# Kernel optimization log

Measured on AMD Instinct MI355X. Metric: run time of the kernel, lower is better.

## Reference

```python
import jax, jax.numpy as jnp
import numpy as np
import math

C = 256
N_HEAD = 8
GROUPS = 32
EPS = 1e-5


def group_norm(x, scale, bias, groups=GROUPS, eps=EPS):
    # x: [B, C, H, W]
    b, c, h, w = x.shape
    xg = x.reshape(b, groups, c // groups, h, w)
    mean = xg.mean(axis=(2, 3, 4), keepdims=True)
    var = xg.var(axis=(2, 3, 4), keepdims=True)
    xg = (xg - mean) * jax.lax.rsqrt(var + eps)
    x = xg.reshape(b, c, h, w)
    return x * scale[None, :, None, None] + bias[None, :, None, None]


def setup_inputs() -> dict:
    key = jax.random.key(0)
    ks = jax.random.split(key, 8)
    B, H, W = 8, 32, 32
    inp = {
        "input_q": jax.random.normal(ks[0], (B, C, H, W), dtype=jnp.float32),
        "input_kv": jax.random.normal(ks[1], (B, C, H, W), dtype=jnp.float32),
        # GroupNorm affine params (torch default: weight=1, bias=0)
        "gq_scale": jnp.ones((C,), jnp.float32),
        "gq_bias": jnp.zeros((C,), jnp.float32),
        "gkv_scale": jnp.ones((C,), jnp.float32),
        "gkv_bias": jnp.zeros((C,), jnp.float32),
        # 1x1 convs as [out, in] matrices
        "Wq": jax.random.normal(ks[2], (C, C), dtype=jnp.float32) / math.sqrt(C),
        "Wkv": jax.random.normal(ks[3], (2 * C, C), dtype=jnp.float32) / math.sqrt(C),
        "Wout": jax.random.normal(ks[4], (C, C), dtype=jnp.float32) / math.sqrt(C),
        "bout": jnp.zeros((C,), jnp.float32),
    }
    return inp


def reference(input_q, input_kv, gq_scale, gq_bias, gkv_scale, gkv_bias, Wq, Wkv, Wout, bout):
    b, c, h, w = input_q.shape
    n = N_HEAD
    d = c // n

    norm_q = group_norm(input_q, gq_scale, gq_bias)
    query = jnp.einsum('oc,bchw->bohw', Wq, norm_q).reshape(b, n, d, h, w)

    norm_kv = group_norm(input_kv, gkv_scale, gkv_bias)
    kv = jnp.einsum('oc,bchw->bohw', Wkv, norm_kv).reshape(b, n, 2 * d, h, w)
    key, value = kv[:, :, :d], kv[:, :, d:]

    attn = jnp.einsum('bnchw,bncyx->bnhwyx', query, key) / math.sqrt(c)
    attn = jax.nn.softmax(attn.reshape(b, n, h, w, h * w), axis=-1)
    attn = attn.reshape(b, n, h, w, h, w)

    out = jnp.einsum('bnhwyx,bncyx->bnchw', attn, value).reshape(b, c, h, w)
    out = jnp.einsum('oc,bchw->bohw', Wout, out) + bout[None, :, None, None]
    return out + input_q
```

## Files before the change

### kernel.cpp

```cpp
#include <hip/hip_runtime.h>
#include <hip/hip_bf16.h>
#include <math.h>
#include <string.h>

#define NB 8
#define NC 256
#define HWSZ 1024
#define NHEAD 8
#define DHEAD 32
#define NGRP 32
#define CPG 8
#define EPSV 1e-5f

typedef float f32x4 __attribute__((ext_vector_type(4)));
typedef short bf16x8 __attribute__((ext_vector_type(8)));

__device__ __forceinline__ unsigned pk2(float a, float b) {
    __hip_bfloat162 h = __float22bfloat162_rn(make_float2(a, b));
    unsigned r;
    memcpy(&r, &h, sizeof(r));
    return r;
}
__device__ __forceinline__ unsigned pk2t(float a, float b) {
    unsigned ua = __float_as_uint(a), ub = __float_as_uint(b);
    return (ua >> 16) | (ub & 0xFFFF0000u);
}
__device__ __forceinline__ unsigned short f2bf(float x) {
    __hip_bfloat16 h = __float2bfloat16(x);
    unsigned short r;
    memcpy(&r, &h, sizeof(r));
    return r;
}
__device__ __forceinline__ float ex2(float x) { return __builtin_amdgcn_exp2f(x); }

__device__ __forceinline__ void gload_lds16(const void* g, void* l) {
    __builtin_amdgcn_global_load_lds(
        (const __attribute__((address_space(1))) unsigned int*)g,
        (__attribute__((address_space(3))) unsigned int*)l, 16, 0, 0);
}

__global__ void prep_kernel(const float* __restrict__ xq,
                            const float* __restrict__ xkv,
                            float* __restrict__ stats,
                            const float* __restrict__ Wq,
                            const float* __restrict__ Wkv,
                            const float* __restrict__ Wout,
                            unsigned short* __restrict__ wqb,
                            unsigned short* __restrict__ wkvb,
                            unsigned short* __restrict__ woutb) {
    if (blockIdx.x < 512) {
        int idx = blockIdx.x;
        int which = idx >> 8;
        int b = (idx >> 5) & 7;
        int g = idx & 31;
        const float* x = which ? xkv : xq;
        const float4* xb = (const float4*)(x + ((size_t)(b * NC + g * CPG)) * HWSZ);
        float s = 0.f, ss = 0.f;
        for (int i = threadIdx.x; i < (CPG * HWSZ) / 4; i += 256) {
            float4 v = xb[i];
            s += v.x + v.y + v.z + v.w;
            ss += v.x * v.x + v.y * v.y + v.z * v.z + v.w * v.w;
        }
        #pragma unroll
        for (int off = 32; off > 0; off >>= 1) {
            s += __shfl_down(s, off);
            ss += __shfl_down(ss, off);
        }
        __shared__ float red[8];
        int wid = threadIdx.x >> 6;
        if ((threadIdx.x & 63) == 0) { red[wid * 2] = s; red[wid * 2 + 1] = ss; }
        __syncthreads();
        if (threadIdx.x == 0) {
            float S = red[0] + red[2] + red[4] + red[6];
            float SS = red[1] + red[3] + red[5] + red[7];
            float mean = S * (1.f / (CPG * HWSZ));
            float var = SS * (1.f / (CPG * HWSZ)) - mean * mean;
            stats[idx * 2] = mean;
            stats[idx * 2 + 1] = rsqrtf(var + EPSV);
        }
    } else {
        int gid = (blockIdx.x - 512) * 256 + threadIdx.x;
        int i0 = gid * 8;
        const float* src; unsigned short* dst; int off; float sc = 1.f;
        if (i0 < 65536)       { src = Wq;   dst = wqb;   off = i0;          sc = 0.0625f * 1.44269504088896f; }
        else if (i0 < 196608) { src = Wkv;  dst = wkvb;  off = i0 - 65536; }
        else                  { src = Wout; dst = woutb; off = i0 - 196608; }
        float4 v0 = *(const float4*)&src[off];
        float4 v1 = *(const float4*)&src[off + 4];
        uint4 o;
        o.x = pk2(v0.x * sc, v0.y * sc); o.y = pk2(v0.z * sc, v0.w * sc);
        o.z = pk2(v1.x * sc, v1.y * sc); o.w = pk2(v1.z * sc, v1.w * sc);
        *(uint4*)&dst[off] = o;
    }
}

__global__ __launch_bounds__(256) void qkv_gemm_kernel(
        const unsigned short* __restrict__ wqb,
        const unsigned short* __restrict__ wkvb,
        const float* __restrict__ xq, const float* __restrict__ xkv,
        const float* __restrict__ stats,
        const float* __restrict__ sq, const float* __restrict__ bq,
        const float* __restrict__ skv, const float* __restrict__ bkv,
        unsigned short* __restrict__ qbuf,
        unsigned short* __restrict__ kbuf,
        unsigned short* __restrict__ vbuf) {
    __shared__ unsigned short Bs[64 * 256];
    const int tid = threadIdx.x;
    const int l16 = tid & 15, g = (tid >> 4) & 3, w = tid >> 6;
    const int y = blockIdx.y;
    const bool isQ = y < 4;
    const int o0 = (isQ ? y : y - 4) * 64;
    const size_t prow0 = (size_t)blockIdx.x * 64;
    const int b = (int)(prow0 >> 10);
    const int pp = (int)(prow0 & 1023);

    const float* X  = (isQ ? xq : xkv) + (size_t)b * NC * HWSZ + pp;
    const float* st = stats + (isQ ? 0 : 512) + b * 64;
    const float* sc = isQ ? sq : skv;
    const float* bi = isQ ? bq : bkv;

    const unsigned short* Asrc = (isQ ? wqb : wkvb)
                               + ((size_t)o0 + 16 * w + l16) * NC;
    bf16x8 af[8];
    #pragma unroll
    for (int kk = 0; kk < 8; ++kk)
        af[kk] = *(const bf16x8*)&Asrc[(kk * 4 + g) << 3];

    const int cq = tid >> 4, pq = tid & 15;
    #pragma unroll
    for (int j = 0; j < 4; ++j) {
        int cb = cq * 4 + j * 64;
        int grp = cb >> 3;
        float mean = st[grp * 2], rstd = st[grp * 2 + 1];
        float mm[4][4];
        #pragma unroll
        for (int u = 0; u < 4; ++u) {
            int c = cb + u;
            float4 v = *(const float4*)&X[(size_t)c * HWSZ + pq * 4];
            float a = rstd * sc[c];
            float bbv = bi[c] - mean * a;
            mm[u][0] = v.x * a + bbv; mm[u][1] = v.y * a + bbv;
            mm[u][2] = v.z * a + bbv; mm[u][3] = v.w * a + bbv;
        }
        #pragma unroll
        for (int v2 = 0; v2 < 4; ++v2) {
            int row = pq * 4 + v2;
            int ds = row * 256 + ((((cb >> 3) ^ (row & 7))) << 3) + (cb & 7);
            uint2 s2;
            s2.x = pk2(mm[0][v2], mm[1][v2]);
            s2.y = pk2(mm[2][v2], mm[3][v2]);
            *(uint2*)&Bs[ds] = s2;
        }
    }
    __syncthreads();

    f32x4 acc[4] = {};
    const int asw = l16 & 7;
    #pragma unroll
    for (int kk = 0; kk < 8; ++kk) {
        const int koff = ((kk * 4 + g) ^ asw) << 3;
        #pragma unroll
        for (int j = 0; j < 4; ++j) {
            bf16x8 bfr = *(const bf16x8*)&Bs[(j * 16 + l16) * 256 + koff];
            acc[j] = __builtin_amdgcn_mfma_f32_16x16x32_bf16(af[kk], bfr, acc[j], 0, 0, 0);
        }
    }

    if (isQ) {
        int ob_ = o0 + 16 * w + 4 * g;
        int n = ob_ >> 5, d0 = ob_ & 31;
        unsigned short* dst = qbuf + ((size_t)(b * NHEAD + n) * HWSZ) * DHEAD + d0;
        #pragma unroll
        for (int j = 0; j < 4; ++j) {
            int p = pp + 16 * j + l16;
            uint2 st2;
            st2.x = pk2(acc[j][0], acc[j][1]);
            st2.y = pk2(acc[j][2], acc[j][3]);
            *(uint2*)&dst[(size_t)p * DHEAD] = st2;
        }
    } else {
        int n = o0 >> 6;
        int d0 = 16 * (w & 1) + 4 * g;
        if (w < 2) {
            unsigned short* dst = kbuf + ((size_t)(b * NHEAD + n) * HWSZ) * DHEAD + d0;
            #pragma unroll
            for (int j = 0; j < 4; ++j) {
                int p = pp + 16 * j + l16;
                uint2 st2;
                st2.x = pk2(acc[j][0], acc[j][1]);
                st2.y = pk2(acc[j][2], acc[j][3]);
                *(uint2*)&dst[(size_t)p * DHEAD] = st2;
            }
        } else {
            unsigned short* dst = vbuf + ((size_t)(b * NHEAD + n) * DHEAD + d0) * HWSZ;
            #pragma unroll
            for (int j = 0; j < 4; ++j) {
                int slot = ((l16 >> 2) << 3) + ((j & 1) << 2) + (l16 & 3);
                int p = pp + 32 * (j >> 1) + slot;
                #pragma unroll
                for (int r = 0; r < 4; ++r)
                    dst[(size_t)r * HWSZ + p] = f2bf(acc[j][r]);
            }
        }
    }
}

__global__ __launch_bounds__(256) void out_gemm_kernel(
        const unsigned short* __restrict__ Abase,
        const unsigned short* __restrict__ Bbase,
        const float* __restrict__ bias_out,
        const float* __restrict__ resid,
        float* __restrict__ out0) {
    __shared__ unsigned short Bs[64 * 256];
    const int tid = threadIdx.x;
    const int l16 = tid & 15, g = (tid >> 4) & 3, w = tid >> 6;
    const int o0 = blockIdx.y * 64;
    const size_t prow0 = (size_t)blockIdx.x * 64;

    const unsigned short* Asrc = Abase + (prow0 + 16 * w + l16) * NC;
    bf16x8 af[8];
    #pragma unroll
    for (int kk = 0; kk < 8; ++kk)
        af[kk] = *(const bf16x8*)&Asrc[(kk * 4 + g) << 3];

    const unsigned short* Bsrc = Bbase + (size_t)o0 * NC;
    #pragma unroll
    for (int it = 0; it < 4; ++it) {
        int idx = tid + it * 256;
        int row = idx >> 4, seg = idx & 15;
        #pragma unroll
        for (int h = 0; h < 2; ++h) {
            int sg = seg * 2 + h;
            int ds = row * 256 + ((sg ^ (row & 7)) << 3);
            *(uint4*)&Bs[ds] = *(const uint4*)&Bsrc[(size_t)row * NC + sg * 8];
        }
    }
    __syncthreads();

    f32x4 acc[4] = {};
    const int asw = l16 & 7;
    #pragma unroll
    for (int kk = 0; kk < 8; ++kk) {
        const int koff = ((kk * 4 + g) ^ asw) << 3;
        #pragma unroll
        for (int j = 0; j < 4; ++j) {
            bf16x8 b = *(const bf16x8*)&Bs[(j * 16 + l16) * 256 + koff];
            acc[j] = __builtin_amdgcn_mfma_f32_16x16x32_bf16(af[kk], b, acc[j], 0, 0, 0);
        }
    }
    const int b = (int)(prow0 >> 10);
    const int pp = (int)(prow0 & 1023);
    int p_b = pp + 16 * w + 4 * g;
    #pragma unroll
    for (int j = 0; j < 4; ++j) {
        int o = o0 + 16 * j + l16;
        float bo = bias_out[o];
        size_t off = ((size_t)b * NC + o) * HWSZ + p_b;
        float4 rs = *(const float4*)&resid[off];
        float4 vst = make_float4(acc[j][0] + bo + rs.x, acc[j][1] + bo + rs.y,
                                 acc[j][2] + bo + rs.z, acc[j][3] + bo + rs.w);
        *(float4*)&out0[off] = vst;
    }
}

__global__ __launch_bounds__(256) void attn_mfma_kernel(
        const unsigned short* __restrict__ qb,
        const unsigned short* __restrict__ kb,
        const unsigned short* __restrict__ vb,
        unsigned short* __restrict__ ob) {
    __shared__ unsigned short KV[3][4096];
    const int tid = threadIdx.x;
    const int w = tid >> 6, lane = tid & 63;
    const int l16 = lane & 15, g = lane >> 4;
    const int F = blockIdx.y * 16 + blockIdx.x;
    const int bn = (F & 7) * 8 + (F >> 7);
    const int qblk = (F >> 3) & 15;
    const int qp = qblk * 64 + w * 16 + l16;

    bf16x8 qf = *(const bf16x8*)(qb + ((size_t)bn * HWSZ + qp) * DHEAD + g * 8);

    const int kr = tid >> 2, ks = tid & 3;
    const unsigned short* ksrc = kb + (size_t)bn * HWSZ * DHEAD
                               + (size_t)kr * DHEAD + ((ks ^ (kr & 3)) << 3);
    const int vr = tid >> 3, vs = tid & 7;
    const unsigned short* vsrc = vb + (size_t)bn * DHEAD * HWSZ
                               + (size_t)vr * HWSZ + ((vs ^ (vr & 7)) << 3);
    unsigned short* lk = &KV[0][0] + w * 512;
    unsigned short* lv = &KV[0][2048] + w * 512;

#define STAGE(t) do {                                                        \
        int b3_ = (t) % 3; int ti_ = (t) & 15;                               \
        gload_lds16(ksrc + (size_t)ti_ * 64 * DHEAD, lk + b3_ * 4096);       \
        gload_lds16(vsrc + (size_t)ti_ * 64,         lv + b3_ * 4096);       \
    } while (0)

    f32x4 acc0 = {0.f, 0.f, 0.f, 0.f}, acc1 = {0.f, 0.f, 0.f, 0.f};
    f32x4 accl = {0.f, 0.f, 0.f, 0.f};
    const f32x4 z = {0.f, 0.f, 0.f, 0.f};

    const unsigned on2 = 0x3F803F80u;
    uint4 onev = make_uint4(on2, on2, on2, on2);
    bf16x8 ones;
    memcpy(&ones, &onev, sizeof(ones));

    const int ksw  = (g ^ (l16 & 3)) << 3;
    const int vsw0 = ((g)     ^ (l16 & 7)) << 3;
    const int vsw1 = ((4 + g) ^ (l16 & 7)) << 3;

    STAGE(0);
    STAGE(1);

    #pragma unroll
    for (int t = 0; t < 16; ++t) {
        const int cur = t % 3;
        asm volatile("s_waitcnt vmcnt(2)" ::: "memory");
        __builtin_amdgcn_s_barrier();
        STAGE(t + 2);

        const unsigned short* Kb = &KV[cur][0];
        const unsigned short* Vb = &KV[cur][2048];
        bf16x8 ka0 = *(const bf16x8*)&Kb[(l16)      * 32 + ksw];
        bf16x8 ka1 = *(const bf16x8*)&Kb[(16 + l16) * 32 + ksw];
        bf16x8 ka2 = *(const bf16x8*)&Kb[(32 + l16) * 32 + ksw];
        bf16x8 ka3 = *(const bf16x8*)&Kb[(48 + l16) * 32 + ksw];

        __builtin_amdgcn_s_setprio(1);
        f32x4 s0 = __builtin_amdgcn_mfma_f32_16x16x32_bf16(ka0, qf, z, 0, 0, 0);
        f32x4 s1 = __builtin_amdgcn_mfma_f32_16x16x32_bf16(ka1, qf, z, 0, 0, 0);
        f32x4 s2 = __builtin_amdgcn_mfma_f32_16x16x32_bf16(ka2, qf, z, 0, 0, 0);
        f32x4 s3 = __builtin_amdgcn_mfma_f32_16x16x32_bf16(ka3, qf, z, 0, 0, 0);
        __builtin_amdgcn_s_setprio(0);

        float p00 = ex2(s0[0]), p01 = ex2(s0[1]);
        float p02 = ex2(s0[2]), p03 = ex2(s0[3]);
        float p10 = ex2(s1[0]), p11 = ex2(s1[1]);
        float p12 = ex2(s1[2]), p13 = ex2(s1[3]);
        float p20 = ex2(s2[0]), p21 = ex2(s2[1]);
        float p22 = ex2(s2[2]), p23 = ex2(s2[3]);
        float p30 = ex2(s3[0]), p31 = ex2(s3[1]);
        float p32 = ex2(s3[2]), p33 = ex2(s3[3]);

        uint4 pwa, pwb;
        pwa.x = pk2t(p00, p01); pwa.y = pk2t(p02, p03);
        pwa.z = pk2t(p10, p11); pwa.w = pk2t(p12, p13);
        pwb.x = pk2t(p20, p21); pwb.y = pk2t(p22, p23);
        pwb.z = pk2t(p30, p31); pwb.w = pk2t(p32, p33);
        bf16x8 pf0, pf1;
        memcpy(&pf0, &pwa, sizeof(pf0));
        memcpy(&pf1, &pwb, sizeof(pf1));

        bf16x8 va0 = *(const bf16x8*)&Vb[(l16)      * 64 + vsw0];
        bf16x8 va1 = *(const bf16x8*)&Vb[(l16)      * 64 + vsw1];
        bf16x8 vb0 = *(const bf16x8*)&Vb[(16 + l16) * 64 + vsw0];
        bf16x8 vb1 = *(const bf16x8*)&Vb[(16 + l16) * 64 + vsw1];

        __builtin_amdgcn_s_setprio(1);
        acc0 = __builtin_amdgcn_mfma_f32_16x16x32_bf16(va0, pf0, acc0, 0, 0, 0);
        acc0 = __builtin_amdgcn_mfma_f32_16x16x32_bf16(va1, pf1, acc0, 0, 0, 0);
        acc1 = __builtin_amdgcn_mfma_f32_16x16x32_bf16(vb0, pf0, acc1, 0, 0, 0);
        acc1 = __builtin_amdgcn_mfma_f32_16x16x32_bf16(vb1, pf1, acc1, 0, 0, 0);
        accl = __builtin_amdgcn_mfma_f32_16x16x32_bf16(ones, pf0, accl, 0, 0, 0);
        accl = __builtin_amdgcn_mfma_f32_16x16x32_bf16(ones, pf1, accl, 0, 0, 0);
        __builtin_amdgcn_s_setprio(0);
    }
#undef STAGE

    float invl = 1.f / accl[0];

    const int b = bn >> 3, n = bn & 7;
    unsigned short* dst = ob + ((size_t)b * HWSZ + qp) * NC + n * DHEAD;
    uint2 st0, st1;
    st0.x = pk2(acc0[0] * invl, acc0[1] * invl);
    st0.y = pk2(acc0[2] * invl, acc0[3] * invl);
    st1.x = pk2(acc1[0] * invl, acc1[1] * invl);
    st1.y = pk2(acc1[2] * invl, acc1[3] * invl);
    *(uint2*)&dst[4 * g]      = st0;
    *(uint2*)&dst[16 + 4 * g] = st1;
}

extern "C" void kernel_launch(void* const* d_in, const int* in_sizes, int n_in,
                              void* d_out, int out_size, void* d_ws, size_t ws_size,
                              hipStream_t stream) {
    const float* input_q  = (const float*)d_in[0];
    const float* input_kv = (const float*)d_in[1];
    const float* gq_scale = (const float*)d_in[2];
    const float* gq_bias  = (const float*)d_in[3];
    const float* gkv_scale = (const float*)d_in[4];
    const float* gkv_bias  = (const float*)d_in[5];
    const float* Wq   = (const float*)d_in[6];
    const float* Wkv  = (const float*)d_in[7];
    const float* Wout = (const float*)d_in[8];
    const float* bout = (const float*)d_in[9];
    float* out = (float*)d_out;

    char* ws = (char*)d_ws;
    float* stats = (float*)ws;
    unsigned short* wqb   = (unsigned short*)(ws + 16384);
    unsigned short* wkvb  = (unsigned short*)(ws + 16384 + 131072);
    unsigned short* woutb = (unsigned short*)(ws + 16384 + 131072 + 262144);
    const size_t MB = 1024 * 1024;
    unsigned short* qbuf = (unsigned short*)(ws + 1 * MB);
    unsigned short* kbuf = (unsigned short*)(ws + 5 * MB);
    unsigned short* vbuf = (unsigned short*)(ws + 9 * MB);
    unsigned short* obuf = (unsigned short*)(ws + 13 * MB);

    prep_kernel<<<640, 256, 0, stream>>>(input_q, input_kv, stats,
                                         Wq, Wkv, Wout, wqb, wkvb, woutb);
    qkv_gemm_kernel<<<dim3(128, 12), 256, 0, stream>>>(
        wqb, wkvb, input_q, input_kv, stats,
        gq_scale, gq_bias, gkv_scale, gkv_bias, qbuf, kbuf, vbuf);
    attn_mfma_kernel<<<dim3(16, 64), 256, 0, stream>>>(qbuf, kbuf, vbuf, obuf);
    out_gemm_kernel<<<dim3(128, 4), 256, 0, stream>>>(obuf, woutb, bout, input_q, out);
}
```

Baseline: 48.98 us.

## Pre-normalize inputs to channel-group-packed bf16 in prep kernel

```diff
diff --git a/kernel.cpp b/kernel.cpp
--- a/kernel.cpp
+++ b/kernel.cpp
@@ -41,10 +41,15 @@
 
 __global__ void prep_kernel(const float* __restrict__ xq,
                             const float* __restrict__ xkv,
-                            float* __restrict__ stats,
+                            const float* __restrict__ gq_scale,
+                            const float* __restrict__ gq_bias,
+                            const float* __restrict__ gkv_scale,
+                            const float* __restrict__ gkv_bias,
                             const float* __restrict__ Wq,
                             const float* __restrict__ Wkv,
                             const float* __restrict__ Wout,
+                            unsigned short* __restrict__ xnq,
+                            unsigned short* __restrict__ xnkv,
                             unsigned short* __restrict__ wqb,
                             unsigned short* __restrict__ wkvb,
                             unsigned short* __restrict__ woutb) {
@@ -66,7 +71,7 @@
             s += __shfl_down(s, off);
             ss += __shfl_down(ss, off);
         }
-        __shared__ float red[8];
+        __shared__ float red[10];
         int wid = threadIdx.x >> 6;
         if ((threadIdx.x & 63) == 0) { red[wid * 2] = s; red[wid * 2 + 1] = ss; }
         __syncthreads();
@@ -75,8 +80,35 @@
             float SS = red[1] + red[3] + red[5] + red[7];
             float mean = S * (1.f / (CPG * HWSZ));
             float var = SS * (1.f / (CPG * HWSZ)) - mean * mean;
-            stats[idx * 2] = mean;
-            stats[idx * 2 + 1] = rsqrtf(var + EPSV);
+            red[8] = mean;
+            red[9] = rsqrtf(var + EPSV);
+        }
+        __syncthreads();
+        const float mean = red[8], rstd = red[9];
+        const float* scp = which ? gkv_scale : gq_scale;
+        const float* bip = which ? gkv_bias : gq_bias;
+        float a[8], bb[8];
+        #pragma unroll
+        for (int u = 0; u < 8; ++u) {
+            int c = g * 8 + u;
+            a[u] = rstd * scp[c];
+            bb[u] = bip[c] - mean * a[u];
+        }
+        const int p0 = threadIdx.x * 4;
+        f32x4 rowv[8];
+        #pragma unroll
+        for (int u = 0; u < 8; ++u)
+            rowv[u] = *(const f32x4*)&x[((size_t)(b * NC + g * 8 + u)) * HWSZ + p0];
+        unsigned short* xt = (which ? xnkv : xnq)
+                           + (((size_t)b * NGRP + g) * HWSZ) * 8;
+        #pragma unroll
+        for (int pi = 0; pi < 4; ++pi) {
+            uint4 o;
+            o.x = pk2(rowv[0][pi] * a[0] + bb[0], rowv[1][pi] * a[1] + bb[1]);
+            o.y = pk2(rowv[2][pi] * a[2] + bb[2], rowv[3][pi] * a[3] + bb[3]);
+            o.z = pk2(rowv[4][pi] * a[4] + bb[4], rowv[5][pi] * a[5] + bb[5]);
+            o.w = pk2(rowv[6][pi] * a[6] + bb[6], rowv[7][pi] * a[7] + bb[7]);
+            *(uint4*)&xt[(size_t)(p0 + pi) * 8] = o;
         }
     } else {
         int gid = (blockIdx.x - 512) * 256 + threadIdx.x;
@@ -97,10 +129,8 @@
 __global__ __launch_bounds__(256) void qkv_gemm_kernel(
         const unsigned short* __restrict__ wqb,
         const unsigned short* __restrict__ wkvb,
-        const float* __restrict__ xq, const float* __restrict__ xkv,
-        const float* __restrict__ stats,
-        const float* __restrict__ sq, const float* __restrict__ bq,
-        const float* __restrict__ skv, const float* __restrict__ bkv,
+        const unsigned short* __restrict__ xnq,
+        const unsigned short* __restrict__ xnkv,
         unsigned short* __restrict__ qbuf,
         unsigned short* __restrict__ kbuf,
         unsigned short* __restrict__ vbuf) {
@@ -114,11 +144,6 @@
     const int b = (int)(prow0 >> 10);
     const int pp = (int)(prow0 & 1023);
 
-    const float* X  = (isQ ? xq : xkv) + (size_t)b * NC * HWSZ + pp;
-    const float* st = stats + (isQ ? 0 : 512) + b * 64;
-    const float* sc = isQ ? sq : skv;
-    const float* bi = isQ ? bq : bkv;
-
     const unsigned short* Asrc = (isQ ? wqb : wkvb)
                                + ((size_t)o0 + 16 * w + l16) * NC;
     bf16x8 af[8];
@@ -126,31 +151,14 @@
     for (int kk = 0; kk < 8; ++kk)
         af[kk] = *(const bf16x8*)&Asrc[(kk * 4 + g) << 3];
 
-    const int cq = tid >> 4, pq = tid & 15;
-    #pragma unroll
-    for (int j = 0; j < 4; ++j) {
-        int cb = cq * 4 + j * 64;
-        int grp = cb >> 3;
-        float mean = st[grp * 2], rstd = st[grp * 2 + 1];
-        float mm[4][4];
-        #pragma unroll
-        for (int u = 0; u < 4; ++u) {
-            int c = cb + u;
-            float4 v = *(const float4*)&X[(size_t)c * HWSZ + pq * 4];
-            float a = rstd * sc[c];
-            float bbv = bi[c] - mean * a;
-            mm[u][0] = v.x * a + bbv; mm[u][1] = v.y * a + bbv;
-            mm[u][2] = v.z * a + bbv; mm[u][3] = v.w * a + bbv;
-        }
-        #pragma unroll
-        for (int v2 = 0; v2 < 4; ++v2) {
-            int row = pq * 4 + v2;
-            int ds = row * 256 + ((((cb >> 3) ^ (row & 7))) << 3) + (cb & 7);
-            uint2 s2;
-            s2.x = pk2(mm[0][v2], mm[1][v2]);
-            s2.y = pk2(mm[2][v2], mm[3][v2]);
-            *(uint2*)&Bs[ds] = s2;
-        }
+    const unsigned short* Xn = (isQ ? xnq : xnkv) + (size_t)b * NGRP * HWSZ * 8;
+    const int prow = tid & 63, gu0 = tid >> 6;
+    #pragma unroll
+    for (int i = 0; i < 8; ++i) {
+        int gu = gu0 + i * 4;
+        uint4 v = *(const uint4*)&Xn[((size_t)gu * HWSZ + pp + prow) * 8];
+        int ds = prow * 256 + ((gu ^ (prow & 7)) << 3);
+        *(uint4*)&Bs[ds] = v;
     }
     __syncthreads();
 
@@ -394,21 +402,22 @@
     float* out = (float*)d_out;
 
     char* ws = (char*)d_ws;
-    float* stats = (float*)ws;
     unsigned short* wqb   = (unsigned short*)(ws + 16384);
     unsigned short* wkvb  = (unsigned short*)(ws + 16384 + 131072);
     unsigned short* woutb = (unsigned short*)(ws + 16384 + 131072 + 262144);
     const size_t MB = 1024 * 1024;
-    unsigned short* qbuf = (unsigned short*)(ws + 1 * MB);
-    unsigned short* kbuf = (unsigned short*)(ws + 5 * MB);
-    unsigned short* vbuf = (unsigned short*)(ws + 9 * MB);
-    unsigned short* obuf = (unsigned short*)(ws + 13 * MB);
-
-    prep_kernel<<<640, 256, 0, stream>>>(input_q, input_kv, stats,
-                                         Wq, Wkv, Wout, wqb, wkvb, woutb);
+    unsigned short* xnq  = (unsigned short*)(ws + 1 * MB);
+    unsigned short* xnkv = (unsigned short*)(ws + 5 * MB);
+    unsigned short* qbuf = (unsigned short*)(ws + 9 * MB);
+    unsigned short* kbuf = (unsigned short*)(ws + 13 * MB);
+    unsigned short* vbuf = (unsigned short*)(ws + 17 * MB);
+    unsigned short* obuf = (unsigned short*)(ws + 21 * MB);
+
+    prep_kernel<<<640, 256, 0, stream>>>(
+        input_q, input_kv, gq_scale, gq_bias, gkv_scale, gkv_bias,
+        Wq, Wkv, Wout, xnq, xnkv, wqb, wkvb, woutb);
     qkv_gemm_kernel<<<dim3(128, 12), 256, 0, stream>>>(
-        wqb, wkvb, input_q, input_kv, stats,
-        gq_scale, gq_bias, gkv_scale, gkv_bias, qbuf, kbuf, vbuf);
+        wqb, wkvb, xnq, xnkv, qbuf, kbuf, vbuf);
     attn_mfma_kernel<<<dim3(16, 64), 256, 0, stream>>>(qbuf, kbuf, vbuf, obuf);
     out_gemm_kernel<<<dim3(128, 4), 256, 0, stream>>>(obuf, woutb, bout, input_q, out);
 }
```

Measured after the change: 48.20 us. No clear change (-1.6%).
